# Kernel tuning notes

Measured on AMD Instinct MI355X. Metric: run time of the kernel, lower is better.

The kernel has to match this reference:

```python
import jax, jax.numpy as jnp
import numpy as np

NEG_INF = float('-inf')


def setup_inputs() -> dict:
    key = jax.random.key(0)
    ks = jax.random.split(key, 5)
    Sq, Sk, H, D, B = 4096, 4096, 8, 128, 4
    q = jax.random.normal(ks[0], (Sq, H, D), jnp.float32)
    k_local = jax.random.normal(ks[1], (Sk, H, D), jnp.float32)
    v_local = jax.random.normal(ks[2], (Sk, H, D), jnp.float32)
    k_remote = jax.random.normal(ks[3], (Sk, H, D), jnp.float32)
    v_remote = jax.random.normal(ks[4], (Sk, H, D), jnp.float32)
    # 4 ragged range pairs: equal blocks of 1024 q-tokens <-> 1024 kv-tokens
    blk = Sq // B
    starts = jnp.arange(B, dtype=jnp.int32) * blk
    ranges = jnp.stack([starts, starts + blk], axis=1)  # [B, 2]
    return dict(
        q=q, k_local=k_local, v_local=v_local,
        k_remote=k_remote, v_remote=v_remote,
        q_ranges_local=ranges, kv_ranges_local=ranges,
        is_causal_local=jnp.ones((B,), bool),
        q_ranges_remote=ranges, kv_ranges_remote=ranges,
        is_causal_remote=jnp.zeros((B,), bool),
    )


def _range_mask(Sq, Sk, q_ranges, kv_ranges, is_causal):
    # Build [Sq, Sk] attend-mask from ragged (q,kv) range pairs.
    qpos = jnp.arange(Sq)[None, :, None]   # [1, Sq, 1]
    kpos = jnp.arange(Sk)[None, None, :]   # [1, 1, Sk]
    qs = q_ranges[:, 0][:, None, None]; qe = q_ranges[:, 1][:, None, None]
    ks = kv_ranges[:, 0][:, None, None]; ke = kv_ranges[:, 1][:, None, None]
    in_q = (qpos >= qs) & (qpos < qe)
    in_k = (kpos >= ks) & (kpos < ke)
    # bottom-right-aligned causal within each range pair
    shift = (ke - ks) - (qe - qs)
    caus = (kpos - ks) <= (qpos - qs) + shift
    m = in_q & in_k & (caus | ~is_causal[:, None, None])  # [B, Sq, Sk]
    return jnp.any(m, axis=0)  # [Sq, Sk]


def _flex_attn(q, k, v, q_ranges, kv_ranges, is_causal):
    # q: [Sq, H, D]; k, v: [Sk, H, D] -> out [Sq, H, D], lse [H, Sq]
    Sq, H, D = q.shape
    Sk = k.shape[0]
    mask = _range_mask(Sq, Sk, q_ranges, kv_ranges, is_causal)  # [Sq, Sk]
    scale = 1.0 / np.sqrt(D).astype(np.float32)
    scores = jnp.einsum('qhd,khd->hqk', q, k) * scale
    scores = jnp.where(mask[None], scores, NEG_INF)
    mx = jnp.max(scores, axis=-1)                      # [H, Sq]
    mx_safe = jnp.where(jnp.isneginf(mx), 0.0, mx)
    e = jnp.where(mask[None], jnp.exp(scores - mx_safe[..., None]), 0.0)
    s = jnp.sum(e, axis=-1)                            # [H, Sq]
    lse = jnp.where(s > 0, mx_safe + jnp.log(jnp.where(s > 0, s, 1.0)), NEG_INF)
    p = e / jnp.where(s > 0, s, 1.0)[..., None]
    out = jnp.einsum('hqk,khd->qhd', p, v)
    return out, lse


def _safe_subtract(a, b):
    both_ninf = (a == b) & jnp.isneginf(a)
    return jnp.where(both_ninf, NEG_INF, a - b)


def _correct_lse(lse1, lse2):
    mn = jnp.minimum(lse1, lse2).astype(jnp.float32)
    mx = jnp.maximum(lse1, lse2).astype(jnp.float32)
    return (mx + jax.nn.softplus(_safe_subtract(mn, mx))).astype(lse1.dtype)


def _correct_out(o1, lse1, o2, lse2, lse):
    # lse*: [H, Sq] -> weights [Sq, H, 1]
    w1 = jnp.exp(_safe_subtract(lse1, lse)).T[..., None].astype(jnp.float32)
    w2 = jnp.exp(_safe_subtract(lse2, lse)).T[..., None].astype(jnp.float32)
    return (w1 * o1 + w2 * o2).astype(o1.dtype)


def _result_correction(out_list, lse_list, overlap_degree):
    # Faithful to the original loop structure (stage 1 merged twice).
    curr_lse = _correct_lse(lse_list[0], lse_list[1])
    curr_out = _correct_out(out_list[0], lse_list[0], out_list[1], lse_list[1], curr_lse)
    for i in range(overlap_degree):
        orig_lse, orig_out = curr_lse, curr_out
        curr_lse = _correct_lse(orig_lse, lse_list[i + 1])
        curr_out = _correct_out(orig_out, orig_lse, out_list[i + 1], lse_list[i + 1], curr_lse)
    return curr_out, curr_lse


def reference(q, k_local, v_local, k_remote, v_remote,
              q_ranges_local, kv_ranges_local, is_causal_local,
              q_ranges_remote, kv_ranges_remote, is_causal_remote):
    o0, l0 = _flex_attn(q, k_local, v_local, q_ranges_local, kv_ranges_local, is_causal_local)
    o1, l1 = _flex_attn(q, k_remote, v_remote, q_ranges_remote, kv_ranges_remote, is_causal_remote)
    out, lse = _result_correction([o0, o1], [l0, l1], overlap_degree=1)
    return out, lse
```

## Files before the change

### kernel.cpp

```cpp
#include <hip/hip_runtime.h>
#include <math.h>


constexpr int NH = 8;
constexpr int DH = 128;
#define NEG_INF (-INFINITY)

typedef __bf16 bf16x8 __attribute__((ext_vector_type(8)));
typedef float  f32x4  __attribute__((ext_vector_type(4)));

__device__ __forceinline__ unsigned short f2bf_rne(float x) {
  union { float f; unsigned u; } v; v.f = x;
  unsigned r = v.u + 0x7FFFu + ((v.u >> 16) & 1u);
  return (unsigned short)(r >> 16);
}
__device__ __forceinline__ unsigned pk2(float lo, float hi) {
  return (unsigned)f2bf_rne(lo) | ((unsigned)f2bf_rne(hi) << 16);
}
__device__ __forceinline__ void gl2lds16(const void* g, void* l) {
  __builtin_amdgcn_global_load_lds(
      (const __attribute__((address_space(1))) unsigned int*)g,
      (__attribute__((address_space(3))) unsigned int*)l, 16, 0, 0);
}
#define MFMA16 __builtin_amdgcn_mfma_f32_16x16x32_bf16

__global__ void kconv(const float* __restrict__ kl, const float* __restrict__ kr,
                      unsigned short* __restrict__ out, int Sk) {
  const float* in = blockIdx.y ? kr : kl;
  unsigned short* o = out + (size_t)blockIdx.y * NH * Sk * DH;
  const int t = threadIdx.x;
  const size_t base = (size_t)blockIdx.x * 4096;
  #pragma unroll
  for (int rdx = 0; rdx < 4; ++rdx) {
    const size_t L = base + rdx * 1024 + (size_t)t * 4;
    float4 f = *(const float4*)(in + L);
    const int kv  = (int)(L >> 10);
    const int rem = (int)(L & 1023);
    const int h = rem >> 7, d = rem & 127;
    const int pe = (((d >> 3) ^ (kv & 7)) << 3) + (d & 7);
    uint2 w = make_uint2(pk2(f.x, f.y), pk2(f.z, f.w));
    *(uint2*)&o[((size_t)h * Sk + kv) * DH + pe] = w;
  }
}

__global__ void vconv(const float* __restrict__ vl, const float* __restrict__ vr,
                      unsigned short* __restrict__ out, int Sk) {
  __shared__ unsigned short T[64 * 132];
  const float* in = blockIdx.z ? vr : vl;
  const int h   = blockIdx.y;
  const int kv0 = blockIdx.x * 64;
  unsigned short* panel =
      out + (((size_t)blockIdx.z * NH + h) * (Sk >> 6) + blockIdx.x) * (DH * 64);
  const int t = threadIdx.x;
  {
    const int off = (t & 31) * 4;
    const int kvr = t >> 5;
    #pragma unroll
    for (int rdx = 0; rdx < 8; ++rdx) {
      const int kv = rdx * 8 + kvr;
      float4 f = *(const float4*)(in + ((size_t)(kv0 + kv) * NH + h) * DH + off);
      *(uint2*)&T[kv * 132 + off] = make_uint2(pk2(f.x, f.y), pk2(f.z, f.w));
    }
  }
  __syncthreads();
  #pragma unroll
  for (int rdx = 0; rdx < 4; ++rdx) {
    const int G = rdx * 256 + t;
    const int d = G >> 3, gphys = G & 7;
    const int gk = gphys ^ (d & 7);
    unsigned short v[8];
    #pragma unroll
    for (int j = 0; j < 8; ++j) v[j] = T[(gk * 8 + j) * 132 + d];
    *(uint4*)&panel[(size_t)G * 8] = *(uint4*)v;
  }
}

__global__ __launch_bounds__(256, 2)
void fa_kernel(const float* __restrict__ qp,
               const unsigned short* __restrict__ Kb,
               const unsigned short* __restrict__ Vt,
               const int* __restrict__ qrl, const int* __restrict__ kvrl,
               const int* __restrict__ czl,
               const int* __restrict__ qrr, const int* __restrict__ kvrr,
               const int* __restrict__ czr,
               float* __restrict__ outp, float* __restrict__ lsep,
               unsigned short* __restrict__ pO, float* __restrict__ pL,
               int Sq, int Sk, int B, int nsplit, int direct)
{
  __shared__ __align__(16) unsigned short Klds[64 * DH];
  __shared__ __align__(16) unsigned short Vlds[DH * 64];
  __shared__ __align__(16) unsigned short Plds[4 * 2048];

  const int tid = threadIdx.x, wave = tid >> 6, lane = tid & 63;
  const int quad = lane >> 4, c = lane & 15;
  const int bid = blockIdx.x;
  const int h   = bid & 7;
  const int nqt = Sq >> 7;
  const int tt  = bid >> 3;
  const int qtile = tt % nqt, split = tt / nqt;
  const int q0 = qtile * 128;
  const int qw = q0 + wave * 32;

  const float kscale = 0.12751743f;

  bf16x8 ones;
  #pragma unroll
  for (int i = 0; i < 8; ++i) ones[i] = (__bf16)1.0f;

  bf16x8 qfrag[2][4];
  #pragma unroll
  for (int s = 0; s < 2; ++s) {
    const float* gq = qp + ((size_t)(qw + s * 16 + c) * NH + h) * DH + quad * 8;
    #pragma unroll
    for (int f = 0; f < 4; ++f) {
      float4 a = *(const float4*)(gq + f * 32);
      float4 b = *(const float4*)(gq + f * 32 + 4);
      uint4 tq = { pk2(a.x,a.y), pk2(a.z,a.w), pk2(b.x,b.y), pk2(b.z,b.w) };
      qfrag[s][f] = __builtin_bit_cast(bf16x8, tq);
    }
  }

  f32x4 accO[2][8];
  #pragma unroll
  for (int s = 0; s < 2; ++s)
    #pragma unroll
    for (int i = 0; i < 8; ++i) accO[s][i] = (f32x4){0.f,0.f,0.f,0.f};
  f32x4 lacc[2] = {(f32x4){0.f,0.f,0.f,0.f}, (f32x4){0.f,0.f,0.f,0.f}};

  for (int src = 0; src < 2; ++src) {
    const unsigned short* kbh = Kb + ((size_t)src * NH + h) * Sk * DH;
    const unsigned short* vth = Vt + ((size_t)src * NH + h) * ((size_t)(Sk >> 6) * DH * 64);
    const int* qr  = src ? qrr : qrl;
    const int* kvr = src ? kvrr : kvrl;
    const int* cz  = src ? czr : czl;
    const float sbias = src ? 1.0f : 0.0f;

    for (int b = 0; b < B; ++b) {
      const int qs = qr[2*b], qe = qr[2*b+1];
      const int ks = kvr[2*b], ke = kvr[2*b+1];
      const int causal = cz[b] != 0;
      if (qe <= q0 || qs >= q0 + 128 || ks >= ke) continue;
      const int shift = (ke - ks) - (qe - qs);
      const int qmaxb = min(q0 + 127, qe - 1);
      const int kendb = causal ? min(ke, ks + (qmaxb - qs) + shift + 1) : ke;

      int wkend = INT_MIN;
      {
        int wqs = max(qw, qs), wqe = min(qw + 32, qe);
        if (wqs < wqe) {
          int wqmax = min(qw + 31, qe - 1);
          wkend = causal ? min(ke, ks + (wqmax - qs) + shift + 1) : ke;
        }
      }

      const int kv_lo = (ks >> 6) << 6;
      for (int kv0 = kv_lo + split * 64; kv0 < kendb; kv0 += nsplit * 64) {
        __syncthreads();
        {
          const char* gk = (const char*)(kbh + (size_t)kv0 * DH) + wave * 4096 + lane * 16;
          char* lk = (char*)Klds + wave * 4096 + lane * 16;
          #pragma unroll
          for (int i = 0; i < 4; ++i) gl2lds16(gk + i * 1024, lk + i * 1024);
          const char* gv = (const char*)(vth + (size_t)(kv0 >> 6) * (DH * 64)) + wave * 4096 + lane * 16;
          char* lv = (char*)Vlds + wave * 4096 + lane * 16;
          #pragma unroll
          for (int i = 0; i < 4; ++i) gl2lds16(gv + i * 1024, lv + i * 1024);
        }
        __syncthreads();

        if (kv0 >= wkend) continue;

        f32x4 sc[2][4];
        #pragma unroll
        for (int s = 0; s < 2; ++s)
          #pragma unroll
          for (int st = 0; st < 4; ++st) sc[s][st] = (f32x4){0.f,0.f,0.f,0.f};
        #pragma unroll
        for (int st = 0; st < 4; ++st) {
          const unsigned short* kr_ = &Klds[(st * 16 + c) * DH];
          #pragma unroll
          for (int f = 0; f < 4; ++f) {
            const int phys = (f * 4 + quad) ^ (c & 7);
            bf16x8 kf = *(const bf16x8*)&kr_[phys * 8];
            sc[0][st] = MFMA16(qfrag[0][f], kf, sc[0][st], 0, 0, 0);
            sc[1][st] = MFMA16(qfrag[1][f], kf, sc[1][st], 0, 0, 0);
          }
        }
        const bool interior = (kv0 >= ks) && (kv0 + 64 <= ke) &&
                              (qw >= qs) && (qw + 32 <= qe) &&
                              (!causal || (kv0 + 63 - ks) <= (qw - qs) + shift);
        if (!interior) {
          #pragma unroll
          for (int s = 0; s < 2; ++s)
            #pragma unroll
            for (int st = 0; st < 4; ++st) {
              const int kvg = kv0 + st * 16 + c;
              const int kin = (kvg >= ks) && (kvg < ke);
              #pragma unroll
              for (int r = 0; r < 4; ++r) {
                const int qg = qw + s * 16 + quad * 4 + r;
                const int ok = kin && (qg >= qs) && (qg < qe) &&
                               (!causal || (kvg - ks) <= (qg - qs) + shift);
                sc[s][st][r] = ok ? sc[s][st][r] : NEG_INF;
              }
            }
        }
        #pragma unroll
        for (int s = 0; s < 2; ++s) {
          unsigned short* pb = &Plds[wave * 2048 + s * 1024];
          #pragma unroll
          for (int st = 0; st < 4; ++st) {
            const int kvi  = (st & 1) * 16 + c;
            const int base = (st >> 1) * 512 + ((kvi >> 3) << 7) + (kvi & 7);
            #pragma unroll
            for (int r = 0; r < 4; ++r) {
              float pv = __builtin_amdgcn_exp2f(sc[s][st][r] * kscale + sbias);
              pb[base + (quad * 4 + r) * 8] =
                  (unsigned short)(__builtin_bit_cast(unsigned, pv) >> 16);
            }
          }
        }
        #pragma unroll
        for (int s = 0; s < 2; ++s) {
          #pragma unroll
          for (int kc = 0; kc < 2; ++kc) {
            bf16x8 pf = *(const bf16x8*)&Plds[wave * 2048 + s * 1024 + kc * 512 + lane * 8];
            lacc[s] = MFMA16(pf, ones, lacc[s], 0, 0, 0);
            #pragma unroll
            for (int dt = 0; dt < 8; ++dt) {
              const int d = dt * 16 + c;
              const int phys = (kc * 4 + quad) ^ (c & 7);
              bf16x8 vf = *(const bf16x8*)&Vlds[d * 64 + phys * 8];
              accO[s][dt] = MFMA16(pf, vf, accO[s][dt], 0, 0, 0);
            }
          }
        }
      }
    }
  }

  if (direct) {
    #pragma unroll
    for (int s = 0; s < 2; ++s)
      #pragma unroll
      for (int r = 0; r < 4; ++r) {
        const float sum = lacc[s][r];
        const float rcp = sum > 0.0f ? 1.0f / sum : 0.0f;
        const int qg = qw + s * 16 + quad * 4 + r;
        #pragma unroll
        for (int dt = 0; dt < 8; ++dt)
          outp[((size_t)qg * NH + h) * DH + dt * 16 + c] = accO[s][dt][r] * rcp;
        if (c == 0)
          lsep[(size_t)h * Sq + qg] =
              sum > 0.0f ? 0.6931471805599453f * __builtin_amdgcn_logf(sum) : NEG_INF;
      }
  } else {
    #pragma unroll
    for (int s = 0; s < 2; ++s)
      #pragma unroll
      for (int r = 0; r < 4; ++r) {
        const int qg = qw + s * 16 + quad * 4 + r;
        if (c == 0) pL[((size_t)split * NH + h) * Sq + qg] = lacc[s][r];
        unsigned short* pr = pO + (((size_t)split * Sq + qg) * NH + h) * DH;
        #pragma unroll
        for (int dt = 0; dt < 8; ++dt)
          pr[dt * 16 + c] = f2bf_rne(accO[s][dt][r]);
      }
  }
}

__global__ void merge_kernel(const unsigned short* __restrict__ pO,
                             const float* __restrict__ pL,
                             float* __restrict__ outp, float* __restrict__ lsep,
                             int Sq, int nsplit) {
  const int row = blockIdx.x * 2 + (threadIdx.x >> 7);
  const int d = threadIdx.x & 127;
  const int q = row >> 3, h = row & 7;
  float s = 0.f, o = 0.f;
  for (int sp = 0; sp < nsplit; ++sp) {
    s += pL[((size_t)sp * NH + h) * Sq + q];
    unsigned u = pO[(((size_t)sp * Sq + q) * NH + h) * DH + d];
    o += __builtin_bit_cast(float, u << 16);
  }
  const float rcp = s > 0.f ? 1.0f / s : 0.f;
  outp[(size_t)row * DH + d] = o * rcp;
  if (d == 0)
    lsep[(size_t)h * Sq + q] =
        s > 0.f ? 0.6931471805599453f * __builtin_amdgcn_logf(s) : NEG_INF;
}

extern "C" void kernel_launch(void* const* d_in, const int* in_sizes, int n_in,
                              void* d_out, int out_size, void* d_ws, size_t ws_size,
                              hipStream_t stream) {
  const float* qp = (const float*)d_in[0];
  const float* kl = (const float*)d_in[1];
  const float* vl = (const float*)d_in[2];
  const float* kr = (const float*)d_in[3];
  const float* vr = (const float*)d_in[4];
  const int* qrl  = (const int*)d_in[5];
  const int* kvrl = (const int*)d_in[6];
  const int* czl  = (const int*)d_in[7];
  const int* qrr  = (const int*)d_in[8];
  const int* kvrr = (const int*)d_in[9];
  const int* czr  = (const int*)d_in[10];

  const int B  = in_sizes[5] / 2;
  const int Sq = in_sizes[0] / (NH * DH);
  const int Sk = in_sizes[1] / (NH * DH);
  float* outp = (float*)d_out;
  float* lsep = outp + (size_t)Sq * NH * DH;

  const size_t TEN  = (size_t)NH * Sk * DH;
  const size_t base = 4 * TEN * sizeof(unsigned short);
  unsigned short* Kb = (unsigned short*)d_ws;
  unsigned short* Vt = Kb + 2 * TEN;

  auto needO = [&](int ns) {
    return (size_t)ns * Sq * NH * DH * 2 + (size_t)ns * NH * Sq * 4;
  };
  int ns; int direct = 0;
  if      (ws_size >= base + needO(2)) ns = 2;
  else if (ws_size >= base + needO(1)) ns = 1;
  else { ns = 1; direct = 1; }
  unsigned short* pO = (unsigned short*)((char*)d_ws + base);
  float* pL = (float*)((char*)d_ws + base + (size_t)ns * Sq * NH * DH * 2);

  kconv<<<dim3(Sk / 4, 2), 256, 0, stream>>>(kl, kr, Kb, Sk);
  vconv<<<dim3(Sk / 64, NH, 2), 256, 0, stream>>>(vl, vr, Vt, Sk);

  fa_kernel<<<dim3(ns * (Sq / 128) * NH), 256, 0, stream>>>(
      qp, Kb, Vt, qrl, kvrl, czl, qrr, kvrr, czr,
      outp, lsep, pO, pL, Sq, Sk, B, ns, direct);

  if (!direct)
    merge_kernel<<<dim3(Sq * NH / 2), 256, 0, stream>>>(pO, pL, outp, lsep, Sq, ns);
}
```

Baseline: 186.8 us.

## Double-buffer K/V tiles, fuse conversion kernels, swizzle P, vectorize merge

The attention loop becomes a flattened tile iterator. The next K/V tile is prefetched into a second LDS buffer while the current one is computed, which removes one barrier per tile and overlaps global-to-LDS loads with MFMA work. The K and V conversion kernels are fused into one launch. The P staging layout gets an XOR swizzle to cut LDS bank conflicts, and s_setprio raises priority around the MFMA sections. Odd splits reverse the q-tile order to balance causal work, and the merge kernel now processes two elements per thread. The doubled LDS use may reduce occupancy.

```diff
diff --git a/kernel.cpp b/kernel.cpp
--- a/kernel.cpp
+++ b/kernel.cpp
@@ -1,5 +1,6 @@
 #include <hip/hip_runtime.h>
 #include <math.h>
+#include <limits.h>
 
 
 constexpr int NH = 8;
@@ -24,56 +25,69 @@
 }
 #define MFMA16 __builtin_amdgcn_mfma_f32_16x16x32_bf16
 
-__global__ void kconv(const float* __restrict__ kl, const float* __restrict__ kr,
-                      unsigned short* __restrict__ out, int Sk) {
-  const float* in = blockIdx.y ? kr : kl;
-  unsigned short* o = out + (size_t)blockIdx.y * NH * Sk * DH;
+__global__ void prep_kernel(const float* __restrict__ kl, const float* __restrict__ kr,
+                            const float* __restrict__ vl, const float* __restrict__ vr,
+                            unsigned short* __restrict__ Kb,
+                            unsigned short* __restrict__ Vt, int Sk) {
+  __shared__ unsigned short T[64 * 132];
+  const int nk = Sk >> 2;
+  const int npan = Sk >> 6;
   const int t = threadIdx.x;
-  const size_t base = (size_t)blockIdx.x * 4096;
-  #pragma unroll
-  for (int rdx = 0; rdx < 4; ++rdx) {
-    const size_t L = base + rdx * 1024 + (size_t)t * 4;
-    float4 f = *(const float4*)(in + L);
-    const int kv  = (int)(L >> 10);
-    const int rem = (int)(L & 1023);
-    const int h = rem >> 7, d = rem & 127;
-    const int pe = (((d >> 3) ^ (kv & 7)) << 3) + (d & 7);
-    uint2 w = make_uint2(pk2(f.x, f.y), pk2(f.z, f.w));
-    *(uint2*)&o[((size_t)h * Sk + kv) * DH + pe] = w;
-  }
-}
-
-__global__ void vconv(const float* __restrict__ vl, const float* __restrict__ vr,
-                      unsigned short* __restrict__ out, int Sk) {
-  __shared__ unsigned short T[64 * 132];
-  const float* in = blockIdx.z ? vr : vl;
-  const int h   = blockIdx.y;
-  const int kv0 = blockIdx.x * 64;
-  unsigned short* panel =
-      out + (((size_t)blockIdx.z * NH + h) * (Sk >> 6) + blockIdx.x) * (DH * 64);
-  const int t = threadIdx.x;
-  {
-    const int off = (t & 31) * 4;
-    const int kvr = t >> 5;
-    #pragma unroll
-    for (int rdx = 0; rdx < 8; ++rdx) {
-      const int kv = rdx * 8 + kvr;
-      float4 f = *(const float4*)(in + ((size_t)(kv0 + kv) * NH + h) * DH + off);
-      *(uint2*)&T[kv * 132 + off] = make_uint2(pk2(f.x, f.y), pk2(f.z, f.w));
-    }
-  }
-  __syncthreads();
-  #pragma unroll
-  for (int rdx = 0; rdx < 4; ++rdx) {
-    const int G = rdx * 256 + t;
-    const int d = G >> 3, gphys = G & 7;
-    const int gk = gphys ^ (d & 7);
-    unsigned short v[8];
-    #pragma unroll
-    for (int j = 0; j < 8; ++j) v[j] = T[(gk * 8 + j) * 132 + d];
-    *(uint4*)&panel[(size_t)G * 8] = *(uint4*)v;
-  }
-}
+  int bid = blockIdx.x;
+
+  if (bid < 2 * nk) {
+    const int src = bid >= nk;
+    const int x = src ? bid - nk : bid;
+    const float* in = src ? kr : kl;
+    unsigned short* o = Kb + (size_t)src * NH * Sk * DH;
+    const size_t base = (size_t)x * 4096;
+    #pragma unroll
+    for (int rdx = 0; rdx < 4; ++rdx) {
+      const size_t L = base + rdx * 1024 + (size_t)t * 4;
+      float4 f = *(const float4*)(in + L);
+      const int kv  = (int)(L >> 10);
+      const int rem = (int)(L & 1023);
+      const int h = rem >> 7, d = rem & 127;
+      const int pe = (((d >> 3) ^ (kv & 7)) << 3) + (d & 7);
+      uint2 w = make_uint2(pk2(f.x, f.y), pk2(f.z, f.w));
+      *(uint2*)&o[((size_t)h * Sk + kv) * DH + pe] = w;
+    }
+  } else {
+    bid -= 2 * nk;
+    const int nv = npan * NH;
+    const int src = bid >= nv;
+    if (src) bid -= nv;
+    const int h = bid / npan;
+    const int x = bid % npan;
+    const float* in = src ? vr : vl;
+    const int kv0 = x * 64;
+    unsigned short* panel =
+        Vt + (((size_t)src * NH + h) * npan + x) * (DH * 64);
+    {
+      const int off = (t & 31) * 4;
+      const int kvr_ = t >> 5;
+      #pragma unroll
+      for (int rdx = 0; rdx < 8; ++rdx) {
+        const int kv = rdx * 8 + kvr_;
+        float4 f = *(const float4*)(in + ((size_t)(kv0 + kv) * NH + h) * DH + off);
+        *(uint2*)&T[kv * 132 + off] = make_uint2(pk2(f.x, f.y), pk2(f.z, f.w));
+      }
+    }
+    __syncthreads();
+    #pragma unroll
+    for (int rdx = 0; rdx < 4; ++rdx) {
+      const int G = rdx * 256 + t;
+      const int d = G >> 3, gphys = G & 7;
+      const int gk = gphys ^ (d & 7);
+      unsigned short v[8];
+      #pragma unroll
+      for (int j = 0; j < 8; ++j) v[j] = T[(gk * 8 + j) * 132 + d];
+      *(uint4*)&panel[(size_t)G * 8] = *(uint4*)v;
+    }
+  }
+}
+
+struct TS { int src, b, kv0, qs, qe, ks, ke, causal, shift, kendb; };
 
 __global__ __launch_bounds__(256, 2)
 void fa_kernel(const float* __restrict__ qp,
@@ -87,8 +101,8 @@
                unsigned short* __restrict__ pO, float* __restrict__ pL,
                int Sq, int Sk, int B, int nsplit, int direct)
 {
-  __shared__ __align__(16) unsigned short Klds[64 * DH];
-  __shared__ __align__(16) unsigned short Vlds[DH * 64];
+  __shared__ __align__(16) unsigned short Klds[2][64 * DH];
+  __shared__ __align__(16) unsigned short Vlds[2][DH * 64];
   __shared__ __align__(16) unsigned short Plds[4 * 2048];
 
   const int tid = threadIdx.x, wave = tid >> 6, lane = tid & 63;
@@ -97,7 +111,9 @@
   const int h   = bid & 7;
   const int nqt = Sq >> 7;
   const int tt  = bid >> 3;
-  const int qtile = tt % nqt, split = tt / nqt;
+  int qtile = tt % nqt;
+  const int split = tt / nqt;
+  if (split & 1) qtile = nqt - 1 - qtile;
   const int q0 = qtile * 128;
   const int qw = q0 + wave * 32;
 
@@ -127,116 +143,152 @@
     for (int i = 0; i < 8; ++i) accO[s][i] = (f32x4){0.f,0.f,0.f,0.f};
   f32x4 lacc[2] = {(f32x4){0.f,0.f,0.f,0.f}, (f32x4){0.f,0.f,0.f,0.f}};
 
-  for (int src = 0; src < 2; ++src) {
-    const unsigned short* kbh = Kb + ((size_t)src * NH + h) * Sk * DH;
-    const unsigned short* vth = Vt + ((size_t)src * NH + h) * ((size_t)(Sk >> 6) * DH * 64);
-    const int* qr  = src ? qrr : qrl;
-    const int* kvr = src ? kvrr : kvrl;
-    const int* cz  = src ? czr : czl;
-    const float sbias = src ? 1.0f : 0.0f;
-
-    for (int b = 0; b < B; ++b) {
-      const int qs = qr[2*b], qe = qr[2*b+1];
-      const int ks = kvr[2*b], ke = kvr[2*b+1];
-      const int causal = cz[b] != 0;
-      if (qe <= q0 || qs >= q0 + 128 || ks >= ke) continue;
-      const int shift = (ke - ks) - (qe - qs);
-      const int qmaxb = min(q0 + 127, qe - 1);
-      const int kendb = causal ? min(ke, ks + (qmaxb - qs) + shift + 1) : ke;
-
-      int wkend = INT_MIN;
-      {
-        int wqs = max(qw, qs), wqe = min(qw + 32, qe);
-        if (wqs < wqe) {
-          int wqmax = min(qw + 31, qe - 1);
-          wkend = causal ? min(ke, ks + (wqmax - qs) + shift + 1) : ke;
+  auto nextTile = [&](TS& t) -> bool {
+    t.kv0 += nsplit * 64;
+    while (t.kv0 >= t.kendb) {
+      ++t.b;
+      if (t.b >= B) {
+        t.b = -1; ++t.src;
+        if (t.src >= 2) return false;
+        t.kendb = INT_MIN; t.kv0 = 0;
+        continue;
+      }
+      const int* qr  = t.src ? qrr : qrl;
+      const int* kvr = t.src ? kvrr : kvrl;
+      const int* cz  = t.src ? czr : czl;
+      t.qs = qr[2*t.b]; t.qe = qr[2*t.b+1];
+      t.ks = kvr[2*t.b]; t.ke = kvr[2*t.b+1];
+      if (t.qe <= q0 || t.qs >= q0 + 128 || t.ks >= t.ke) {
+        t.kendb = INT_MIN; t.kv0 = 0; continue;
+      }
+      t.causal = cz[t.b] != 0;
+      t.shift = (t.ke - t.ks) - (t.qe - t.qs);
+      const int qmaxb = min(q0 + 127, t.qe - 1);
+      t.kendb = t.causal ? min(t.ke, t.ks + (qmaxb - t.qs) + t.shift + 1) : t.ke;
+      t.kv0 = ((t.ks >> 6) << 6) + split * 64;
+    }
+    return true;
+  };
+
+  auto stageTile = [&](const TS& t, int bi) {
+    const unsigned short* kbh = Kb + ((size_t)t.src * NH + h) * (size_t)Sk * DH;
+    const char* gk = (const char*)(kbh + (size_t)t.kv0 * DH) + wave * 4096 + lane * 16;
+    char* lk = (char*)&Klds[bi][0] + wave * 4096 + lane * 16;
+    #pragma unroll
+    for (int i = 0; i < 4; ++i) gl2lds16(gk + i * 1024, lk + i * 1024);
+    const unsigned short* vth = Vt + ((size_t)t.src * NH + h) * ((size_t)(Sk >> 6) * DH * 64);
+    const char* gv = (const char*)(vth + (size_t)(t.kv0 >> 6) * (DH * 64)) + wave * 4096 + lane * 16;
+    char* lv = (char*)&Vlds[bi][0] + wave * 4096 + lane * 16;
+    #pragma unroll
+    for (int i = 0; i < 4; ++i) gl2lds16(gv + i * 1024, lv + i * 1024);
+  };
+
+  const int pswz = (lane ^ ((lane >> 3) & 7)) * 8;
+
+  TS cur; cur.src = 0; cur.b = -1; cur.kv0 = 0; cur.kendb = INT_MIN;
+  cur.qs = 0; cur.qe = 0; cur.ks = 0; cur.ke = 0; cur.causal = 0; cur.shift = 0;
+  bool haveCur = nextTile(cur);
+  if (haveCur) stageTile(cur, 0);
+  __syncthreads();
+  int buf = 0;
+
+  while (haveCur) {
+    TS nxt = cur;
+    const bool haveNxt = nextTile(nxt);
+    if (haveNxt) stageTile(nxt, buf ^ 1);
+
+    int wkend = INT_MIN;
+    {
+      const int wqs = max(qw, cur.qs), wqe = min(qw + 32, cur.qe);
+      if (wqs < wqe) {
+        const int wqmax = min(qw + 31, cur.qe - 1);
+        wkend = cur.causal
+              ? min(cur.ke, cur.ks + (wqmax - cur.qs) + cur.shift + 1)
+              : cur.ke;
+      }
+    }
+
+    if (cur.kv0 < wkend) {
+      const int kv0 = cur.kv0, ks = cur.ks, ke = cur.ke;
+      const int qs = cur.qs, qe = cur.qe, causal = cur.causal, shift = cur.shift;
+      const float sbias = cur.src ? 1.0f : 0.0f;
+
+      f32x4 sc[2][4];
+      #pragma unroll
+      for (int s = 0; s < 2; ++s)
+        #pragma unroll
+        for (int st = 0; st < 4; ++st) sc[s][st] = (f32x4){0.f,0.f,0.f,0.f};
+      __builtin_amdgcn_s_setprio(1);
+      #pragma unroll
+      for (int st = 0; st < 4; ++st) {
+        const unsigned short* kr_ = &Klds[buf][(st * 16 + c) * DH];
+        #pragma unroll
+        for (int f = 0; f < 4; ++f) {
+          const int phys = (f * 4 + quad) ^ (c & 7);
+          bf16x8 kf = *(const bf16x8*)&kr_[phys * 8];
+          sc[0][st] = MFMA16(qfrag[0][f], kf, sc[0][st], 0, 0, 0);
+          sc[1][st] = MFMA16(qfrag[1][f], kf, sc[1][st], 0, 0, 0);
         }
       }
-
-      const int kv_lo = (ks >> 6) << 6;
-      for (int kv0 = kv_lo + split * 64; kv0 < kendb; kv0 += nsplit * 64) {
-        __syncthreads();
-        {
-          const char* gk = (const char*)(kbh + (size_t)kv0 * DH) + wave * 4096 + lane * 16;
-          char* lk = (char*)Klds + wave * 4096 + lane * 16;
-          #pragma unroll
-          for (int i = 0; i < 4; ++i) gl2lds16(gk + i * 1024, lk + i * 1024);
-          const char* gv = (const char*)(vth + (size_t)(kv0 >> 6) * (DH * 64)) + wave * 4096 + lane * 16;
-          char* lv = (char*)Vlds + wave * 4096 + lane * 16;
-          #pragma unroll
-          for (int i = 0; i < 4; ++i) gl2lds16(gv + i * 1024, lv + i * 1024);
-        }
-        __syncthreads();
-
-        if (kv0 >= wkend) continue;
-
-        f32x4 sc[2][4];
+      __builtin_amdgcn_s_setprio(0);
+
+      const bool interior = (kv0 >= ks) && (kv0 + 64 <= ke) &&
+                            (qw >= qs) && (qw + 32 <= qe) &&
+                            (!causal || (kv0 + 63 - ks) <= (qw - qs) + shift);
+      if (!interior) {
         #pragma unroll
         for (int s = 0; s < 2; ++s)
           #pragma unroll
-          for (int st = 0; st < 4; ++st) sc[s][st] = (f32x4){0.f,0.f,0.f,0.f};
+          for (int st = 0; st < 4; ++st) {
+            const int kvg = kv0 + st * 16 + c;
+            const int kin = (kvg >= ks) && (kvg < ke);
+            #pragma unroll
+            for (int r = 0; r < 4; ++r) {
+              const int qg = qw + s * 16 + quad * 4 + r;
+              const int ok = kin && (qg >= qs) && (qg < qe) &&
+                             (!causal || (kvg - ks) <= (qg - qs) + shift);
+              sc[s][st][r] = ok ? sc[s][st][r] : NEG_INF;
+            }
+          }
+      }
+      #pragma unroll
+      for (int s = 0; s < 2; ++s) {
+        unsigned short* pb = &Plds[wave * 2048 + s * 1024];
         #pragma unroll
         for (int st = 0; st < 4; ++st) {
-          const unsigned short* kr_ = &Klds[(st * 16 + c) * DH];
+          const int kvi = (st & 1) * 16 + c;
+          const int xv  = (((kvi >> 3) << 1) | (quad >> 1)) & 7;
+          const int gb  = ((kvi >> 3) << 4) + quad * 4;
+          const int cb  = (st >> 1) * 512 + (kvi & 7);
           #pragma unroll
-          for (int f = 0; f < 4; ++f) {
-            const int phys = (f * 4 + quad) ^ (c & 7);
-            bf16x8 kf = *(const bf16x8*)&kr_[phys * 8];
-            sc[0][st] = MFMA16(qfrag[0][f], kf, sc[0][st], 0, 0, 0);
-            sc[1][st] = MFMA16(qfrag[1][f], kf, sc[1][st], 0, 0, 0);
+          for (int r = 0; r < 4; ++r) {
+            float pv = __builtin_amdgcn_exp2f(sc[s][st][r] * kscale + sbias);
+            pb[cb + ((gb + r) ^ xv) * 8] =
+                (unsigned short)(__builtin_bit_cast(unsigned, pv) >> 16);
           }
         }
-        const bool interior = (kv0 >= ks) && (kv0 + 64 <= ke) &&
-                              (qw >= qs) && (qw + 32 <= qe) &&
-                              (!causal || (kv0 + 63 - ks) <= (qw - qs) + shift);
-        if (!interior) {
+      }
+      __builtin_amdgcn_s_setprio(1);
+      #pragma unroll
+      for (int s = 0; s < 2; ++s) {
+        #pragma unroll
+        for (int kc = 0; kc < 2; ++kc) {
+          bf16x8 pf = *(const bf16x8*)&Plds[wave * 2048 + s * 1024 + kc * 512 + pswz];
+          lacc[s] = MFMA16(pf, ones, lacc[s], 0, 0, 0);
           #pragma unroll
-          for (int s = 0; s < 2; ++s)
-            #pragma unroll
-            for (int st = 0; st < 4; ++st) {
-              const int kvg = kv0 + st * 16 + c;
-              const int kin = (kvg >= ks) && (kvg < ke);
-              #pragma unroll
-              for (int r = 0; r < 4; ++r) {
-                const int qg = qw + s * 16 + quad * 4 + r;
-                const int ok = kin && (qg >= qs) && (qg < qe) &&
-                               (!causal || (kvg - ks) <= (qg - qs) + shift);
-                sc[s][st][r] = ok ? sc[s][st][r] : NEG_INF;
-              }
-            }
-        }
-        #pragma unroll
-        for (int s = 0; s < 2; ++s) {
-          unsigned short* pb = &Plds[wave * 2048 + s * 1024];
-          #pragma unroll
-          for (int st = 0; st < 4; ++st) {
-            const int kvi  = (st & 1) * 16 + c;
-            const int base = (st >> 1) * 512 + ((kvi >> 3) << 7) + (kvi & 7);
-            #pragma unroll
-            for (int r = 0; r < 4; ++r) {
-              float pv = __builtin_amdgcn_exp2f(sc[s][st][r] * kscale + sbias);
-              pb[base + (quad * 4 + r) * 8] =
-                  (unsigned short)(__builtin_bit_cast(unsigned, pv) >> 16);
-            }
+          for (int dt = 0; dt < 8; ++dt) {
+            const int d = dt * 16 + c;
+            const int phys = (kc * 4 + quad) ^ (c & 7);
+            bf16x8 vf = *(const bf16x8*)&Vlds[buf][d * 64 + phys * 8];
+            accO[s][dt] = MFMA16(pf, vf, accO[s][dt], 0, 0, 0);
           }
         }
-        #pragma unroll
-        for (int s = 0; s < 2; ++s) {
-          #pragma unroll
-          for (int kc = 0; kc < 2; ++kc) {
-            bf16x8 pf = *(const bf16x8*)&Plds[wave * 2048 + s * 1024 + kc * 512 + lane * 8];
-            lacc[s] = MFMA16(pf, ones, lacc[s], 0, 0, 0);
-            #pragma unroll
-            for (int dt = 0; dt < 8; ++dt) {
-              const int d = dt * 16 + c;
-              const int phys = (kc * 4 + quad) ^ (c & 7);
-              bf16x8 vf = *(const bf16x8*)&Vlds[d * 64 + phys * 8];
-              accO[s][dt] = MFMA16(pf, vf, accO[s][dt], 0, 0, 0);
-            }
-          }
-        }
-      }
-    }
+      }
+      __builtin_amdgcn_s_setprio(0);
+    }
+
+    __syncthreads();
+    cur = nxt; haveCur = haveNxt; buf ^= 1;
   }
 
   if (direct) {
@@ -273,18 +325,20 @@
                              const float* __restrict__ pL,
                              float* __restrict__ outp, float* __restrict__ lsep,
                              int Sq, int nsplit) {
-  const int row = blockIdx.x * 2 + (threadIdx.x >> 7);
-  const int d = threadIdx.x & 127;
+  const int t = threadIdx.x;
+  const int row = blockIdx.x * 4 + (t >> 6);
+  const int dp = t & 63;
   const int q = row >> 3, h = row & 7;
-  float s = 0.f, o = 0.f;
+  float s = 0.f, o0 = 0.f, o1 = 0.f;
   for (int sp = 0; sp < nsplit; ++sp) {
     s += pL[((size_t)sp * NH + h) * Sq + q];
-    unsigned u = pO[(((size_t)sp * Sq + q) * NH + h) * DH + d];
-    o += __builtin_bit_cast(float, u << 16);
+    unsigned u = *(const unsigned*)&pO[(((size_t)sp * Sq + q) * NH + h) * DH + dp * 2];
+    o0 += __builtin_bit_cast(float, u << 16);
+    o1 += __builtin_bit_cast(float, u & 0xffff0000u);
   }
   const float rcp = s > 0.f ? 1.0f / s : 0.f;
-  outp[(size_t)row * DH + d] = o * rcp;
-  if (d == 0)
+  *(float2*)&outp[(size_t)row * DH + dp * 2] = make_float2(o0 * rcp, o1 * rcp);
+  if (dp == 0)
     lsep[(size_t)h * Sq + q] =
         s > 0.f ? 0.6931471805599453f * __builtin_amdgcn_logf(s) : NEG_INF;
 }
@@ -325,13 +379,13 @@
   unsigned short* pO = (unsigned short*)((char*)d_ws + base);
   float* pL = (float*)((char*)d_ws + base + (size_t)ns * Sq * NH * DH * 2);
 
-  kconv<<<dim3(Sk / 4, 2), 256, 0, stream>>>(kl, kr, Kb, Sk);
-  vconv<<<dim3(Sk / 64, NH, 2), 256, 0, stream>>>(vl, vr, Vt, Sk);
+  const int prep_blocks = 2 * (Sk / 4) + 2 * (Sk / 64) * NH;
+  prep_kernel<<<dim3(prep_blocks), 256, 0, stream>>>(kl, kr, vl, vr, Kb, Vt, Sk);
 
   fa_kernel<<<dim3(ns * (Sq / 128) * NH), 256, 0, stream>>>(
       qp, Kb, Vt, qrl, kvrl, czl, qrr, kvrr, czr,
       outp, lsep, pO, pL, Sq, Sk, B, ns, direct);
 
   if (!direct)
-    merge_kernel<<<dim3(Sq * NH / 2), 256, 0, stream>>>(pO, pL, outp, lsep, Sq, ns);
-}
+    merge_kernel<<<dim3(Sq * NH / 4), 256, 0, stream>>>(pO, pL, outp, lsep, Sq, ns);
+}
```

Measured after the change: 179.9 us. 3.7% less time.
